# Kernel optimization log

Hardware: AMD Instinct MI355X
Metric: run time of the kernel (lower is better)

The kernel has to match this reference:

```python
import jax, jax.numpy as jnp
import numpy as np

NUM_HEADS = 16
WINDOW_SIZE = 256  # config.window_size; layer is 'local'


def setup_inputs() -> dict:
    key = jax.random.key(0)
    ks = jax.random.split(key, 8)
    B, S, H = 4, 2048, 1024
    scale = 1.0 / np.sqrt(H)
    return {
        "x": jax.random.normal(ks[0], (B, S, H), dtype=jnp.float32),
        "x_clean": jax.random.normal(ks[1], (B, S, H), dtype=jnp.float32),
        "ablation_mask": jax.random.uniform(ks[2], (B, S, H), dtype=jnp.float32),
        "Wq": jax.random.normal(ks[3], (H, H), dtype=jnp.float32) * scale,
        "Wk": jax.random.normal(ks[4], (H, H), dtype=jnp.float32) * scale,
        "Wv": jax.random.normal(ks[5], (H, H), dtype=jnp.float32) * scale,
        "Wo": jax.random.normal(ks[6], (H, H), dtype=jnp.float32) * scale,
        "bo": jnp.zeros((H,), dtype=jnp.float32),
    }


def reference(x, x_clean, ablation_mask, Wq, Wk, Wv, Wo, bo):
    B, S, H = x.shape
    nh, hd = NUM_HEADS, H // NUM_HEADS

    def proj(inp, W):  # torch Linear: inp @ W.T -> split heads -> [B, nh, S, hd]
        return jnp.einsum('bsh,oh->bso', inp, W).reshape(B, S, nh, hd).transpose(0, 2, 1, 3)

    q = proj(x, Wq)
    k = proj(x_clean, Wk)
    v = proj(x_clean, Wv)

    # NOTE: original applies NO 1/sqrt(head_dim) scaling.
    scores = jnp.einsum('bnsd,bntd->bnst', q, k)  # [B, nh, S, S]

    i = jnp.arange(S)[:, None]
    j = jnp.arange(S)[None, :]
    # local mask: forbid future (j > i) OR too-far past (j <= i - window)
    masked = (j > i) | (j <= i - WINDOW_SIZE)
    scores = jnp.where(masked[None, None, :, :], -jnp.inf, scores)

    attn = jax.nn.softmax(scores, axis=-1)
    context = jnp.einsum('bnst,bntd->bnsd', attn, v)          # [B, nh, S, hd]
    context = context.transpose(0, 2, 1, 3).reshape(B, S, H)   # merge heads
    context = context * ablation_mask
    return jnp.einsum('bsh,oh->bso', context, Wo) + bo
```

## Files before the change

### kernel.cpp

```cpp
#include <hip/hip_runtime.h>
#include <hip/hip_bf16.h>
#include <cstddef>

#define SB 4
#define SS 2048
#define SH 1024
#define NH 16
#define HD 64
#define WIN 256

typedef __attribute__((ext_vector_type(8))) short bf16x8;
typedef __attribute__((ext_vector_type(8))) _Float16 f16x8;
typedef __attribute__((ext_vector_type(2))) __fp16 fp16v2;
typedef __attribute__((ext_vector_type(4))) float f32x4;

static __device__ __forceinline__ ushort2 pk_bf16(float a, float b) {
    __hip_bfloat162 h = __float22bfloat162_rn(make_float2(a, b));
    union { __hip_bfloat162 h2; ushort2 u2; } u;
    u.h2 = h;
    return u.u2;
}
static __device__ __forceinline__ unsigned short pk1(float a) {
    return pk_bf16(a, 0.f).x;
}

static __device__ __forceinline__ void async16(const void* gptr, void* lptr) {
    __builtin_amdgcn_global_load_lds(
        (const __attribute__((address_space(1))) unsigned int*)gptr,
        (__attribute__((address_space(3))) unsigned int*)lptr, 16, 0, 0);
}

__global__ __launch_bounds__(256) void cvt_all(
    const float* __restrict__ x,  const float* __restrict__ xc,
    const float* __restrict__ Wq, const float* __restrict__ Wk,
    const float* __restrict__ Wv, const float* __restrict__ Wo,
    _Float16* __restrict__ xh,  _Float16* __restrict__ xch,
    _Float16* __restrict__ Wqh, _Float16* __restrict__ Wkh,
    _Float16* __restrict__ Wvh, _Float16* __restrict__ Woh)
{
    const int I4 = SB * SS * SH / 4;
    const int W4 = SH * SH / 4;
    int idx = blockIdx.x * 256 + threadIdx.x;
    const float* src;
    _Float16* dst;
    int off;
    if (idx < I4) { src = x; dst = xh; off = idx; }
    else if (idx < 2 * I4) { src = xc; dst = xch; off = idx - I4; }
    else {
        int r = idx - 2 * I4;
        int wi = r >> 18;
        off = r & (W4 - 1);
        src = (wi == 0) ? Wq : (wi == 1) ? Wk : (wi == 2) ? Wv : Wo;
        dst = (wi == 0) ? Wqh : (wi == 1) ? Wkh : (wi == 2) ? Wvh : Woh;
    }
    float4 v = ((const float4*)src)[off];
    union { fp16v2 h[2]; uint2 u; } t;
    t.h[0] = __builtin_amdgcn_cvt_pkrtz(v.x, v.y);
    t.h[1] = __builtin_amdgcn_cvt_pkrtz(v.z, v.w);
    ((uint2*)dst)[off] = t.u;
}

template<int OUTM>
__global__ __launch_bounds__(256) void gemm4(
    const _Float16* __restrict__ A, const _Float16* __restrict__ W,
    const float* __restrict__ bias, void* __restrict__ C1v,
    int M, int N, int K)
{
    __shared__ __align__(16) unsigned short smem[(OUTM == 2) ? 8704 : 8192];
    _Float16* Ah = (_Float16*)smem;
    _Float16* Bh = (_Float16*)smem + 4096;

    const int tid = threadIdx.x;
    const int m0 = blockIdx.x * 128;
    const int n0 = blockIdx.y * 128;
    const int wave = tid >> 6;
    const int lane = tid & 63;
    const int wm = (wave & 1) * 64;
    const int wn = (wave >> 1) * 64;
    const int lrow = lane & 15;
    const int lk8 = (lane >> 4) * 8;
    const int rq = (lane >> 4) * 4;

    f32x4 acc[4][4];
#pragma unroll
    for (int i = 0; i < 4; ++i)
#pragma unroll
        for (int j = 0; j < 4; ++j)
            acc[i][j] = (f32x4){0.f, 0.f, 0.f, 0.f};

    for (int k0 = 0; k0 < K; k0 += 32) {
        __syncthreads();
#pragma unroll
        for (int u = 0; u < 2; ++u) {
            int reg = u * 4 + wave;
            int slot = reg * 64 + lane;
            int row = slot >> 2;
            int k8 = (slot & 3) * 8;
            async16(A + (size_t)(m0 + row) * K + k0 + k8, Ah + reg * 512);
            async16(W + (size_t)(n0 + row) * K + k0 + k8, Bh + reg * 512);
        }
        __syncthreads();

        f16x8 bf[4];
#pragma unroll
        for (int j = 0; j < 4; ++j)
            bf[j] = *(const f16x8*)&Bh[(wn + j * 16 + lrow) * 32 + lk8];
#pragma unroll
        for (int i = 0; i < 4; ++i) {
            f16x8 af = *(const f16x8*)&Ah[(wm + i * 16 + lrow) * 32 + lk8];
#pragma unroll
            for (int j = 0; j < 4; ++j)
                acc[i][j] = __builtin_amdgcn_mfma_f32_16x16x32_f16(af, bf[j], acc[i][j], 0, 0, 0);
        }
    }

    if (OUTM == 0) {
        float* C = (float*)C1v;
#pragma unroll
        for (int i = 0; i < 4; ++i) {
            int rbase = m0 + wm + i * 16 + rq;
#pragma unroll
            for (int j = 0; j < 4; ++j) {
                int col = n0 + wn + j * 16 + lrow;
                float badd = bias[col];
#pragma unroll
                for (int r = 0; r < 4; ++r)
                    C[(size_t)(rbase + r) * N + col] = acc[i][j][r] + badd;
            }
        }
    } else if (OUTM == 1) {
        _Float16* C = (_Float16*)C1v;
#pragma unroll
        for (int i = 0; i < 4; ++i) {
            int rbase = m0 + wm + i * 16 + rq;
#pragma unroll
            for (int j = 0; j < 4; ++j) {
                int col = n0 + wn + j * 16 + lrow;
#pragma unroll
                for (int r = 0; r < 4; ++r)
                    C[(size_t)(rbase + r) * N + col] = (_Float16)acc[i][j][r];
            }
        }
    } else {
        unsigned short* Ct = (unsigned short*)C1v;
        unsigned short* T = smem;
#pragma unroll
        for (int p = 0; p < 2; ++p) {
            __syncthreads();
            if (wn == p * 64) {
#pragma unroll
                for (int i = 0; i < 4; ++i) {
                    int mloc = wm + i * 16 + rq;
#pragma unroll
                    for (int j = 0; j < 4; ++j) {
                        int cl = j * 16 + lrow;
                        *(ushort4*)&T[cl * 136 + mloc] = make_ushort4(
                            pk1(acc[i][j][0]), pk1(acc[i][j][1]),
                            pk1(acc[i][j][2]), pk1(acc[i][j][3]));
                    }
                }
            }
            __syncthreads();
#pragma unroll
            for (int u = 0; u < 4; ++u) {
                int slot = u * 256 + tid;
                int cl = slot >> 4;
                int m8 = (slot & 15) * 8;
                *(uint4*)(Ct + (size_t)(n0 + p * 64 + cl) * M + m0 + m8) =
                    *(const uint4*)&T[cl * 136 + m8];
            }
        }
    }
}

__global__ __launch_bounds__(256) void attn2(
    const _Float16* Qg, const _Float16* __restrict__ Kg,
    const unsigned short* __restrict__ Vtg, const float* __restrict__ amask,
    _Float16* ctxg)
{
    __shared__ __align__(16) _Float16 K_s[2 * 64 * 32];
    __shared__ __align__(16) unsigned short Vt_s[2 * 64 * 32];
    __shared__ __align__(16) unsigned short P_s[128 * 72];

    const int t = threadIdx.x;
    const int qb = blockIdx.x, h = blockIdx.y, b = blockIdx.z;
    const int t0 = qb * 128;
    const int wave = t >> 6, lane = t & 63;
    const int lrow = lane & 15;
    const int lk8 = (lane >> 4) * 8;
    const int wq = wave * 32;
    const int rq = (lane >> 4) * 4;
    const int M = SB * SS;

    f16x8 qf[2][2];
#pragma unroll
    for (int i = 0; i < 2; ++i)
#pragma unroll
        for (int ki = 0; ki < 2; ++ki)
            qf[i][ki] = *(const f16x8*)(Qg +
                (size_t)(b * SS + t0 + wq + i * 16 + lrow) * SH + h * HD + ki * 32 + lk8);

    f32x4 o[2][4];
    float lsum[2][4];
#pragma unroll
    for (int i = 0; i < 2; ++i)
#pragma unroll
        for (int j = 0; j < 4; ++j) o[i][j] = (f32x4){0.f, 0.f, 0.f, 0.f};
#pragma unroll
    for (int i = 0; i < 2; ++i)
#pragma unroll
        for (int r = 0; r < 4; ++r) lsum[i][r] = 0.f;

    int cl = t0 - (WIN - 1);
    cl = cl < 0 ? 0 : cl;
    const int c_lo = cl >> 6;
    const int c_hi = (t0 >> 6) + 1;

    for (int c = c_lo; c <= c_hi; ++c) {
        const int key0 = c * 64;
        __syncthreads();
#pragma unroll
        for (int ki = 0; ki < 2; ++ki) {
            int slot = wave * 64 + lane;
            int row = slot >> 2;
            int e8 = (slot & 3) * 8;
            async16(Kg + (size_t)(b * SS + key0 + row) * SH + h * HD + ki * 32 + e8,
                    (_Float16*)K_s + ki * 2048 + wave * 512);
            async16(Vtg + (size_t)(h * HD + row) * M + b * SS + key0 + ki * 32 + e8,
                    (unsigned short*)Vt_s + ki * 2048 + wave * 512);
        }
        __syncthreads();

        f32x4 s[2][4];
#pragma unroll
        for (int i = 0; i < 2; ++i)
#pragma unroll
            for (int j = 0; j < 4; ++j) s[i][j] = (f32x4){0.f, 0.f, 0.f, 0.f};
#pragma unroll
        for (int ki = 0; ki < 2; ++ki) {
#pragma unroll
            for (int j = 0; j < 4; ++j) {
                f16x8 bh = *(const f16x8*)&K_s[ki * 2048 + (j * 16 + lrow) * 32 + lk8];
#pragma unroll
                for (int i = 0; i < 2; ++i)
                    s[i][j] = __builtin_amdgcn_mfma_f32_16x16x32_f16(qf[i][ki], bh, s[i][j], 0, 0, 0);
            }
        }

#pragma unroll
        for (int i = 0; i < 2; ++i)
#pragma unroll
            for (int j = 0; j < 4; ++j) {
                int jg = key0 + j * 16 + lrow;
#pragma unroll
                for (int r = 0; r < 4; ++r) {
                    int qg = t0 + wq + i * 16 + rq + r;
                    float p = (jg <= qg && jg > qg - WIN) ? __expf(s[i][j][r]) : 0.f;
                    lsum[i][r] += p;
                    P_s[(wq + i * 16 + rq + r) * 72 + j * 16 + lrow] = pk1(p);
                }
            }

#pragma unroll
        for (int ki = 0; ki < 2; ++ki) {
            bf16x8 pf[2];
#pragma unroll
            for (int i = 0; i < 2; ++i)
                pf[i] = *(const bf16x8*)&P_s[(wq + i * 16 + lrow) * 72 + ki * 32 + lk8];
#pragma unroll
            for (int j = 0; j < 4; ++j) {
                bf16x8 vf = *(const bf16x8*)&Vt_s[ki * 2048 + (j * 16 + lrow) * 32 + lk8];
#pragma unroll
                for (int i = 0; i < 2; ++i)
                    o[i][j] = __builtin_amdgcn_mfma_f32_16x16x32_bf16(pf[i], vf, o[i][j], 0, 0, 0);
            }
        }
    }

#pragma unroll
    for (int i = 0; i < 2; ++i)
#pragma unroll
        for (int r = 0; r < 4; ++r) {
#pragma unroll
            for (int m = 1; m < 16; m <<= 1)
                lsum[i][r] += __shfl_xor(lsum[i][r], m);
        }

#pragma unroll
    for (int i = 0; i < 2; ++i)
#pragma unroll
        for (int r = 0; r < 4; ++r) {
            float inv = 1.f / lsum[i][r];
            size_t rowb = (size_t)(b * SS + t0 + wq + i * 16 + rq + r) * SH + h * HD;
#pragma unroll
            for (int j = 0; j < 4; ++j) {
                int d = j * 16 + lrow;
                float msk = amask[rowb + d];
                ctxg[rowb + d] = (_Float16)(o[i][j][r] * inv * msk);
            }
        }
}

extern "C" void kernel_launch(void* const* d_in, const int* in_sizes, int n_in,
                              void* d_out, int out_size, void* d_ws, size_t ws_size,
                              hipStream_t stream)
{
    const float* x     = (const float*)d_in[0];
    const float* xc    = (const float*)d_in[1];
    const float* amask = (const float*)d_in[2];
    const float* Wq    = (const float*)d_in[3];
    const float* Wk    = (const float*)d_in[4];
    const float* Wv    = (const float*)d_in[5];
    const float* Wo    = (const float*)d_in[6];
    const float* bo    = (const float*)d_in[7];
    float* out = (float*)d_out;

    const int M = SB * SS;
    const size_t BUF = (size_t)M * SH;
    const size_t WBUF = (size_t)SH * SH;
    _Float16* xh  = (_Float16*)d_ws;
    _Float16* xch = xh + BUF;
    _Float16* Qh  = xch + BUF;
    _Float16* Kh  = Qh + BUF;
    unsigned short* Vt = (unsigned short*)(Kh + BUF);
    _Float16* Wqh = (_Float16*)(Vt + BUF);
    _Float16* Wkh = Wqh + WBUF;
    _Float16* Wvh = Wkh + WBUF;
    _Float16* Woh = Wvh + WBUF;
    _Float16* ctx = Qh;

    const int total4 = 2 * (M * SH / 4) + 4 * (SH * SH / 4);
    hipLaunchKernelGGL(cvt_all, dim3(total4 / 256), dim3(256), 0, stream,
                       x, xc, Wq, Wk, Wv, Wo, xh, xch, Wqh, Wkh, Wvh, Woh);

    dim3 gg(M / 128, SH / 128);
    dim3 gb(256);
    hipLaunchKernelGGL((gemm4<1>), gg, gb, 0, stream, xh,  Wqh, bo, (void*)Qh, M, SH, SH);
    hipLaunchKernelGGL((gemm4<1>), gg, gb, 0, stream, xch, Wkh, bo, (void*)Kh, M, SH, SH);
    hipLaunchKernelGGL((gemm4<2>), gg, gb, 0, stream, xch, Wvh, bo, (void*)Vt, M, SH, SH);

    hipLaunchKernelGGL(attn2, dim3(SS / 128, NH, SB), dim3(256), 0, stream,
                       Qh, Kh, Vt, amask, ctx);

    hipLaunchKernelGGL((gemm4<0>), gg, gb, 0, stream, ctx, Woh, bo, (void*)out, M, SH, SH);
}
```

Baseline: 309.7 us.

## Deepen GEMM K-step to 64 and restructure attention into per-wave register loads

The GEMM kernels now stage a 64-wide K slice per iteration, which halves the number of barrier pairs per tile at the cost of doubling shared memory. The attention kernel moves to 128-thread blocks of 64 queries. Each wave loads K and V fragments straight from global memory into registers instead of staging them in shared memory, so the block-wide syncs go away and each wave only visits the key chunks its own 32 queries need. The epilogue now goes through shared memory to apply the ablation mask with vectorized float4 loads and 16-byte stores, at the cost of redundant global K/V reads across waves.

After: 304.4 us. No clear change (-1.7%).

```diff
diff --git a/kernel.cpp b/kernel.cpp
--- a/kernel.cpp
+++ b/kernel.cpp
@@ -61,14 +61,14 @@
 }
 
 template<int OUTM>
-__global__ __launch_bounds__(256) void gemm4(
+__global__ __launch_bounds__(256) void gemm5(
     const _Float16* __restrict__ A, const _Float16* __restrict__ W,
     const float* __restrict__ bias, void* __restrict__ C1v,
     int M, int N, int K)
 {
-    __shared__ __align__(16) unsigned short smem[(OUTM == 2) ? 8704 : 8192];
+    __shared__ __align__(16) unsigned short smem[2 * 128 * 64];
     _Float16* Ah = (_Float16*)smem;
-    _Float16* Bh = (_Float16*)smem + 4096;
+    _Float16* Bh = (_Float16*)smem + 8192;
 
     const int tid = threadIdx.x;
     const int m0 = blockIdx.x * 128;
@@ -88,29 +88,36 @@
         for (int j = 0; j < 4; ++j)
             acc[i][j] = (f32x4){0.f, 0.f, 0.f, 0.f};
 
-    for (int k0 = 0; k0 < K; k0 += 32) {
+    for (int k0 = 0; k0 < K; k0 += 64) {
         __syncthreads();
 #pragma unroll
-        for (int u = 0; u < 2; ++u) {
-            int reg = u * 4 + wave;
-            int slot = reg * 64 + lane;
-            int row = slot >> 2;
-            int k8 = (slot & 3) * 8;
-            async16(A + (size_t)(m0 + row) * K + k0 + k8, Ah + reg * 512);
-            async16(W + (size_t)(n0 + row) * K + k0 + k8, Bh + reg * 512);
-        }
+        for (int ki = 0; ki < 2; ++ki)
+#pragma unroll
+            for (int u = 0; u < 2; ++u) {
+                int reg = u * 4 + wave;
+                int slot = reg * 64 + lane;
+                int row = slot >> 2;
+                int k8 = (slot & 3) * 8;
+                async16(A + (size_t)(m0 + row) * K + k0 + ki * 32 + k8,
+                        Ah + ki * 4096 + reg * 512);
+                async16(W + (size_t)(n0 + row) * K + k0 + ki * 32 + k8,
+                        Bh + ki * 4096 + reg * 512);
+            }
         __syncthreads();
 
-        f16x8 bf[4];
-#pragma unroll
-        for (int j = 0; j < 4; ++j)
-            bf[j] = *(const f16x8*)&Bh[(wn + j * 16 + lrow) * 32 + lk8];
-#pragma unroll
-        for (int i = 0; i < 4; ++i) {
-            f16x8 af = *(const f16x8*)&Ah[(wm + i * 16 + lrow) * 32 + lk8];
-#pragma unroll
-            for (int j = 0; j < 4; ++j)
-                acc[i][j] = __builtin_amdgcn_mfma_f32_16x16x32_f16(af, bf[j], acc[i][j], 0, 0, 0);
+#pragma unroll
+        for (int ki = 0; ki < 2; ++ki) {
+            f16x8 bf[4];
+#pragma unroll
+            for (int j = 0; j < 4; ++j)
+                bf[j] = *(const f16x8*)&Bh[ki * 4096 + (wn + j * 16 + lrow) * 32 + lk8];
+#pragma unroll
+            for (int i = 0; i < 4; ++i) {
+                f16x8 af = *(const f16x8*)&Ah[ki * 4096 + (wm + i * 16 + lrow) * 32 + lk8];
+#pragma unroll
+                for (int j = 0; j < 4; ++j)
+                    acc[i][j] = __builtin_amdgcn_mfma_f32_16x16x32_f16(af, bf[j], acc[i][j], 0, 0, 0);
+            }
         }
     }
 
@@ -173,24 +180,22 @@
     }
 }
 
-__global__ __launch_bounds__(256) void attn2(
+__global__ __launch_bounds__(128) void attn3(
     const _Float16* Qg, const _Float16* __restrict__ Kg,
     const unsigned short* __restrict__ Vtg, const float* __restrict__ amask,
     _Float16* ctxg)
 {
-    __shared__ __align__(16) _Float16 K_s[2 * 64 * 32];
-    __shared__ __align__(16) unsigned short Vt_s[2 * 64 * 32];
-    __shared__ __align__(16) unsigned short P_s[128 * 72];
+    __shared__ __align__(16) unsigned short P_s[2][32 * 72];
 
     const int t = threadIdx.x;
-    const int qb = blockIdx.x, h = blockIdx.y, b = blockIdx.z;
-    const int t0 = qb * 128;
     const int wave = t >> 6, lane = t & 63;
+    const int h = blockIdx.y, b = blockIdx.z;
+    const int wq = blockIdx.x * 64 + wave * 32;
     const int lrow = lane & 15;
     const int lk8 = (lane >> 4) * 8;
-    const int wq = wave * 32;
     const int rq = (lane >> 4) * 4;
     const int M = SB * SS;
+    unsigned short* P = P_s[wave];
 
     f16x8 qf[2][2];
 #pragma unroll
@@ -198,7 +203,7 @@
 #pragma unroll
         for (int ki = 0; ki < 2; ++ki)
             qf[i][ki] = *(const f16x8*)(Qg +
-                (size_t)(b * SS + t0 + wq + i * 16 + lrow) * SH + h * HD + ki * 32 + lk8);
+                (size_t)(b * SS + wq + i * 16 + lrow) * SH + h * HD + ki * 32 + lk8);
 
     f32x4 o[2][4];
     float lsum[2][4];
@@ -211,25 +216,21 @@
 #pragma unroll
         for (int r = 0; r < 4; ++r) lsum[i][r] = 0.f;
 
-    int cl = t0 - (WIN - 1);
+    int cl = wq - (WIN - 1);
     cl = cl < 0 ? 0 : cl;
     const int c_lo = cl >> 6;
-    const int c_hi = (t0 >> 6) + 1;
+    const int c_hi = (wq + 31) >> 6;
 
     for (int c = c_lo; c <= c_hi; ++c) {
         const int key0 = c * 64;
-        __syncthreads();
-#pragma unroll
-        for (int ki = 0; ki < 2; ++ki) {
-            int slot = wave * 64 + lane;
-            int row = slot >> 2;
-            int e8 = (slot & 3) * 8;
-            async16(Kg + (size_t)(b * SS + key0 + row) * SH + h * HD + ki * 32 + e8,
-                    (_Float16*)K_s + ki * 2048 + wave * 512);
-            async16(Vtg + (size_t)(h * HD + row) * M + b * SS + key0 + ki * 32 + e8,
-                    (unsigned short*)Vt_s + ki * 2048 + wave * 512);
-        }
-        __syncthreads();
+
+        f16x8 kf[2][4];
+#pragma unroll
+        for (int ki = 0; ki < 2; ++ki)
+#pragma unroll
+            for (int j = 0; j < 4; ++j)
+                kf[ki][j] = *(const f16x8*)(Kg +
+                    (size_t)(b * SS + key0 + j * 16 + lrow) * SH + h * HD + ki * 32 + lk8);
 
         f32x4 s[2][4];
 #pragma unroll
@@ -237,15 +238,12 @@
 #pragma unroll
             for (int j = 0; j < 4; ++j) s[i][j] = (f32x4){0.f, 0.f, 0.f, 0.f};
 #pragma unroll
-        for (int ki = 0; ki < 2; ++ki) {
-#pragma unroll
-            for (int j = 0; j < 4; ++j) {
-                f16x8 bh = *(const f16x8*)&K_s[ki * 2048 + (j * 16 + lrow) * 32 + lk8];
+        for (int ki = 0; ki < 2; ++ki)
+#pragma unroll
+            for (int j = 0; j < 4; ++j)
 #pragma unroll
                 for (int i = 0; i < 2; ++i)
-                    s[i][j] = __builtin_amdgcn_mfma_f32_16x16x32_f16(qf[i][ki], bh, s[i][j], 0, 0, 0);
-            }
-        }
+                    s[i][j] = __builtin_amdgcn_mfma_f32_16x16x32_f16(qf[i][ki], kf[ki][j], s[i][j], 0, 0, 0);
 
 #pragma unroll
         for (int i = 0; i < 2; ++i)
@@ -254,26 +252,32 @@
                 int jg = key0 + j * 16 + lrow;
 #pragma unroll
                 for (int r = 0; r < 4; ++r) {
-                    int qg = t0 + wq + i * 16 + rq + r;
+                    int qg = wq + i * 16 + rq + r;
                     float p = (jg <= qg && jg > qg - WIN) ? __expf(s[i][j][r]) : 0.f;
                     lsum[i][r] += p;
-                    P_s[(wq + i * 16 + rq + r) * 72 + j * 16 + lrow] = pk1(p);
+                    P[(i * 16 + rq + r) * 72 + j * 16 + lrow] = pk1(p);
                 }
             }
+
+        bf16x8 vf[2][4];
+#pragma unroll
+        for (int ki = 0; ki < 2; ++ki)
+#pragma unroll
+            for (int j = 0; j < 4; ++j)
+                vf[ki][j] = *(const bf16x8*)(Vtg +
+                    (size_t)(h * HD + j * 16 + lrow) * M + b * SS + key0 + ki * 32 + lk8);
 
 #pragma unroll
         for (int ki = 0; ki < 2; ++ki) {
             bf16x8 pf[2];
 #pragma unroll
             for (int i = 0; i < 2; ++i)
-                pf[i] = *(const bf16x8*)&P_s[(wq + i * 16 + lrow) * 72 + ki * 32 + lk8];
-#pragma unroll
-            for (int j = 0; j < 4; ++j) {
-                bf16x8 vf = *(const bf16x8*)&Vt_s[ki * 2048 + (j * 16 + lrow) * 32 + lk8];
+                pf[i] = *(const bf16x8*)&P[(i * 16 + lrow) * 72 + ki * 32 + lk8];
+#pragma unroll
+            for (int j = 0; j < 4; ++j)
 #pragma unroll
                 for (int i = 0; i < 2; ++i)
-                    o[i][j] = __builtin_amdgcn_mfma_f32_16x16x32_bf16(pf[i], vf, o[i][j], 0, 0, 0);
-            }
+                    o[i][j] = __builtin_amdgcn_mfma_f32_16x16x32_bf16(pf[i], vf[ki][j], o[i][j], 0, 0, 0);
         }
     }
 
@@ -286,19 +290,36 @@
                 lsum[i][r] += __shfl_xor(lsum[i][r], m);
         }
 
+    _Float16* Pf = (_Float16*)P;
 #pragma unroll
     for (int i = 0; i < 2; ++i)
 #pragma unroll
         for (int r = 0; r < 4; ++r) {
             float inv = 1.f / lsum[i][r];
-            size_t rowb = (size_t)(b * SS + t0 + wq + i * 16 + rq + r) * SH + h * HD;
-#pragma unroll
-            for (int j = 0; j < 4; ++j) {
-                int d = j * 16 + lrow;
-                float msk = amask[rowb + d];
-                ctxg[rowb + d] = (_Float16)(o[i][j][r] * inv * msk);
-            }
-        }
+#pragma unroll
+            for (int j = 0; j < 4; ++j)
+                Pf[(i * 16 + rq + r) * 72 + j * 16 + lrow] = (_Float16)(o[i][j][r] * inv);
+        }
+#pragma unroll
+    for (int u = 0; u < 4; ++u) {
+        int slot = u * 64 + lane;
+        int ro = slot >> 3;
+        int d8 = (slot & 7) * 8;
+        f16x8 v = *(const f16x8*)&Pf[ro * 72 + d8];
+        size_t g = (size_t)(b * SS + wq + ro) * SH + h * HD + d8;
+        float4 ma = *(const float4*)(amask + g);
+        float4 mb = *(const float4*)(amask + g + 4);
+        f16x8 rs;
+        rs[0] = (_Float16)((float)v[0] * ma.x);
+        rs[1] = (_Float16)((float)v[1] * ma.y);
+        rs[2] = (_Float16)((float)v[2] * ma.z);
+        rs[3] = (_Float16)((float)v[3] * ma.w);
+        rs[4] = (_Float16)((float)v[4] * mb.x);
+        rs[5] = (_Float16)((float)v[5] * mb.y);
+        rs[6] = (_Float16)((float)v[6] * mb.z);
+        rs[7] = (_Float16)((float)v[7] * mb.w);
+        *(f16x8*)(ctxg + g) = rs;
+    }
 }
 
 extern "C" void kernel_launch(void* const* d_in, const int* in_sizes, int n_in,
@@ -335,12 +356,12 @@
 
     dim3 gg(M / 128, SH / 128);
     dim3 gb(256);
-    hipLaunchKernelGGL((gemm4<1>), gg, gb, 0, stream, xh,  Wqh, bo, (void*)Qh, M, SH, SH);
-    hipLaunchKernelGGL((gemm4<1>), gg, gb, 0, stream, xch, Wkh, bo, (void*)Kh, M, SH, SH);
-    hipLaunchKernelGGL((gemm4<2>), gg, gb, 0, stream, xch, Wvh, bo, (void*)Vt, M, SH, SH);
-
-    hipLaunchKernelGGL(attn2, dim3(SS / 128, NH, SB), dim3(256), 0, stream,
+    hipLaunchKernelGGL((gemm5<1>), gg, gb, 0, stream, xh,  Wqh, bo, (void*)Qh, M, SH, SH);
+    hipLaunchKernelGGL((gemm5<1>), gg, gb, 0, stream, xch, Wkh, bo, (void*)Kh, M, SH, SH);
+    hipLaunchKernelGGL((gemm5<2>), gg, gb, 0, stream, xch, Wvh, bo, (void*)Vt, M, SH, SH);
+
+    hipLaunchKernelGGL(attn3, dim3(SS / 64, NH, SB), dim3(128), 0, stream,
                        Qh, Kh, Vt, amask, ctx);
 
-    hipLaunchKernelGGL((gemm4<0>), gg, gb, 0, stream, ctx, Woh, bo, (void*)out, M, SH, SH);
-}
+    hipLaunchKernelGGL((gemm5<0>), gg, gb, 0, stream, ctx, Woh, bo, (void*)out, M, SH, SH);
+}
```
